# Kernel tuning notes

Measured on AMD Instinct MI355X. Metric: run time of the kernel, lower is better.

Reference implementation:

```python
import jax, jax.numpy as jnp
import numpy as np

N_NODES = 50000
N_FEAT = 128
HIDDEN = 3
N_EDGES = 600000
N_POWERS = 3


def setup_inputs() -> dict:
    key = jax.random.key(0)
    ks = jax.random.split(key, 6)
    x = jax.random.normal(ks[0], (N_NODES, N_FEAT), dtype=jnp.float32)
    edge_index = jax.random.randint(ks[1], (N_POWERS, 2, N_EDGES), 0, N_NODES, dtype=jnp.int64)
    # MLP params for the 3 adjacency powers, stacked on the leading axis.
    # torch Linear(in,out) stored transposed here: y = x @ W + b.
    Wa = jax.random.normal(ks[2], (N_POWERS, N_FEAT, HIDDEN), dtype=jnp.float32) * (1.0 / np.sqrt(N_FEAT))
    ba = jax.random.normal(ks[3], (N_POWERS, HIDDEN), dtype=jnp.float32) * 0.01
    Wb = jax.random.normal(ks[4], (N_POWERS, HIDDEN, 1), dtype=jnp.float32) * (1.0 / np.sqrt(HIDDEN))
    bb = jax.random.normal(ks[5], (N_POWERS, 1), dtype=jnp.float32) * 0.01
    return {"x": x, "edge_index": edge_index, "Wa": Wa, "ba": ba, "Wb": Wb, "bb": bb}


def reference(x, edge_index, Wa, ba, Wb, bb):
    # Gather source/target node features per edge, per adjacency power.
    x_j = x[edge_index[:, 0]]          # [P, E, F]
    x_i = x[edge_index[:, 1]]          # [P, E, F]
    abs_dif = jnp.abs(x_j - x_i)       # [P, E, F]
    # Tiny per-edge MLP: Linear -> ReLU -> Linear -> Sigmoid (separate params per power).
    h = jax.nn.relu(jnp.einsum('pef,pfh->peh', abs_dif, Wa) + ba[:, None, :])  # [P, E, H]
    w = jax.nn.sigmoid(jnp.einsum('peh,pho->peo', h, Wb) + bb[:, None, :])     # [P, E, 1]
    return w[..., 0]                   # [P, E] edge weights for each power
```

## Files before the change

kernel.cpp:

```cpp
#include <hip/hip_runtime.h>
#include <math.h>

#define N_NODES 50000
#define N_FEAT  128
#define N_EDGES 600000
#define N_POWERS 3

#define PAIRS 5
#define EDGES_PER_BLK (64 * PAIRS)

#define NB64 64
#define CAP64 10240
#define CHUNK 2048
#define NCHUNK 293

typedef _Float16 half2v __attribute__((ext_vector_type(2)));
union HU { unsigned u; half2v h; };

__device__ __forceinline__ int bj_of(int j) { return j / 6250; }

__global__ __launch_bounds__(256) void conv_x_plain(const float* __restrict__ x,
                                                    unsigned* __restrict__ xh,
                                                    const float* __restrict__ Wa,
                                                    unsigned* __restrict__ wah,
                                                    int* __restrict__ cur) {
    const int t = blockIdx.x * 256 + threadIdx.x;
    const float4* x4 = (const float4*)x;
    float4 a = x4[(size_t)t * 2];
    float4 b = x4[(size_t)t * 2 + 1];
    HU p0, p1, p2, p3;
    p0.h = half2v{(_Float16)a.x, (_Float16)a.y};
    p1.h = half2v{(_Float16)a.z, (_Float16)a.w};
    p2.h = half2v{(_Float16)b.x, (_Float16)b.y};
    p3.h = half2v{(_Float16)b.z, (_Float16)b.w};
    ((uint4*)xh)[t] = uint4{p0.u, p1.u, p2.u, p3.u};
    if (blockIdx.x == 0 && threadIdx.x < 192) {
        const int tt = threadIdx.x;
        #pragma unroll
        for (int q = 0; q < 3; ++q) {
            int idx = tt + q * 192;
            int c  = idx % 3;
            int pk = idx / 3;
            int k  = pk % 64;
            int p  = pk / 64;
            float w0 = Wa[p * 384 + (2 * k) * 3 + c];
            float w1 = Wa[p * 384 + (2 * k + 1) * 3 + c];
            HU u; u.h = half2v{(_Float16)w0, (_Float16)w1};
            wah[idx] = u.u;
        }
    }
    if (cur != nullptr && blockIdx.x == 1 && threadIdx.x < N_POWERS * NB64)
        cur[threadIdx.x] = 0;
}

__global__ __launch_bounds__(256) void scatter_onepass(const int* __restrict__ edge_index,
                                                       unsigned long long* __restrict__ su,
                                                       int* __restrict__ cur) {
    __shared__ int tot[4][NB64];
    __shared__ int sh_w[4][NB64];
    __shared__ int sh_lbase[NB64];
    __shared__ int sh_delta[NB64];
    __shared__ int sh_vt;
    __shared__ unsigned long long pay[CHUNK];
    __shared__ int dlt[CHUNK];

    const int p = blockIdx.y, chunk = blockIdx.x;
    const int tid  = threadIdx.x;
    const int lane = tid & 63;
    const int wave = tid >> 6;
    const int* ej = edge_index + (size_t)p * 2 * N_EDGES;
    const int* ei = ej + N_EDGES;
    const int base = chunk * CHUNK;

    int jj[8], ii[8], sbk[8], off[8];
    int run = 0;
    #pragma unroll
    for (int k = 0; k < 8; ++k) {
        const int e = base + k * 256 + tid;
        const bool valid = e < N_EDGES;
        jj[k] = __builtin_nontemporal_load(ej + (valid ? e : 0));
        ii[k] = __builtin_nontemporal_load(ei + (valid ? e : 0));
        const int b = bj_of(jj[k]) * 8 + bj_of(ii[k]);
        sbk[k] = b;
        const unsigned long long m0 = __ballot(b & 1);
        const unsigned long long m1 = __ballot(b & 2);
        const unsigned long long m2 = __ballot(b & 4);
        const unsigned long long m3 = __ballot(b & 8);
        const unsigned long long m4 = __ballot(b & 16);
        const unsigned long long m5 = __ballot(b & 32);
        const unsigned long long vm = __ballot(valid);
        unsigned long long m = ((b & 1) ? m0 : ~m0);
        m &= ((b & 2)  ? m1 : ~m1);
        m &= ((b & 4)  ? m2 : ~m2);
        m &= ((b & 8)  ? m3 : ~m3);
        m &= ((b & 16) ? m4 : ~m4);
        m &= ((b & 32) ? m5 : ~m5);
        m &= vm;
        const int rank = (int)__popcll(m & ((1ull << lane) - 1ull));
        unsigned long long mm = ((lane & 1) ? m0 : ~m0);
        mm &= ((lane & 2)  ? m1 : ~m1);
        mm &= ((lane & 4)  ? m2 : ~m2);
        mm &= ((lane & 8)  ? m3 : ~m3);
        mm &= ((lane & 16) ? m4 : ~m4);
        mm &= ((lane & 32) ? m5 : ~m5);
        mm &= vm;
        const int cnt = (int)__popcll(mm);
        const int pre = __shfl(run, b, 64);
        off[k] = pre + rank;
        run += cnt;
    }
    tot[wave][lane] = run;
    __syncthreads();

    if (tid < NB64) {
        const int t0 = tot[0][tid], t1 = tot[1][tid], t2 = tot[2][tid], t3 = tot[3][tid];
        const int bt = t0 + t1 + t2 + t3;
        int s = bt;
        #pragma unroll
        for (int d = 1; d < 64; d <<= 1) {
            int u = __shfl_up(s, d, 64);
            if (tid >= d) s += u;
        }
        const int lb = s - bt;
        const int g  = atomicAdd(&cur[p * NB64 + tid], bt);
        sh_lbase[tid] = lb;
        sh_delta[tid] = (p * NB64 + tid) * CAP64 + g - lb;
        sh_w[0][tid] = 0;
        sh_w[1][tid] = t0;
        sh_w[2][tid] = t0 + t1;
        sh_w[3][tid] = t0 + t1 + t2;
        if (tid == 63) sh_vt = lb + bt;
    }
    __syncthreads();

    #pragma unroll
    for (int k = 0; k < 8; ++k) {
        const int e = base + k * 256 + tid;
        if (e < N_EDGES) {
            const int b = sbk[k];
            const int pos = sh_lbase[b] + sh_w[wave][b] + off[k];
            pay[pos] = (unsigned long long)(unsigned)(jj[k] | (ii[k] << 16))
                     | ((unsigned long long)e << 32);
            dlt[pos] = sh_delta[b];
        }
    }
    __syncthreads();

    const int vt = sh_vt;
    #pragma unroll
    for (int k = 0; k < 8; ++k) {
        const int pos = k * 256 + tid;
        if (pos < vt)
            su[(size_t)(dlt[pos] + pos)] = pay[pos];
    }
}

template<int PAT>
__device__ __forceinline__ float swz(float v) {
    return __int_as_float(__builtin_amdgcn_ds_swizzle(__float_as_int(v), PAT));
}

__device__ __forceinline__ void dot3_8(const uint4& qa0, const uint4& qa1,
                                       const uint4& qb0, const uint4& qb1,
                                       const HU wa[8][3],
                                       float& h0, float& h1, float& h2) {
    unsigned ua[8] = {qa0.x, qa0.y, qa0.z, qa0.w, qa1.x, qa1.y, qa1.z, qa1.w};
    unsigned ub[8] = {qb0.x, qb0.y, qb0.z, qb0.w, qb1.x, qb1.y, qb1.z, qb1.w};
    h0 = 0.f; h1 = 0.f; h2 = 0.f;
    #pragma unroll
    for (int k = 0; k < 8; ++k) {
        HU a, b, d;
        a.u = ua[k]; b.u = ub[k];
        d.h = a.h - b.h;
        d.u &= 0x7fff7fffu;
        h0 = __builtin_amdgcn_fdot2(d.h, wa[k][0].h, h0, false);
        h1 = __builtin_amdgcn_fdot2(d.h, wa[k][1].h, h1, false);
        h2 = __builtin_amdgcn_fdot2(d.h, wa[k][2].h, h2, false);
    }
}

__global__ __launch_bounds__(256, 4) void adj_kernel_sorted(
    const unsigned* __restrict__ xh,
    const unsigned long long* __restrict__ su,
    const int* __restrict__ cur,
    const unsigned* __restrict__ wah,
    const float* __restrict__ ba,
    const float* __restrict__ Wb,
    const float* __restrict__ bb,
    float* __restrict__ out)
{
    const int p    = blockIdx.y;
    const int bj   = blockIdx.x & 7;
    const int k    = (blockIdx.x >> 3) & 31;
    const int bi   = blockIdx.x >> 8;
    const int sb   = bj * 8 + bi;
    const int tid  = threadIdx.x;
    const int lane = tid & 63;
    const int wave = tid >> 6;
    const int sub  = lane & 7;
    const int grp  = lane >> 3;

    const int count = cur[p * NB64 + sb];
    const int base  = k * EDGES_PER_BLK;
    if (base >= count) return;

    HU wa[8][3];
    {
        const unsigned* wp = wah + ((size_t)p * 64 + sub * 8) * 3;
        #pragma unroll
        for (int kk = 0; kk < 8; ++kk) {
            wa[kk][0].u = wp[kk * 3 + 0];
            wa[kk][1].u = wp[kk * 3 + 1];
            wa[kk][2].u = wp[kk * 3 + 2];
        }
        #pragma unroll
        for (int kk = 0; kk < 8; ++kk) {
            asm volatile("" : "+v"(wa[kk][0].u), "+v"(wa[kk][1].u), "+v"(wa[kk][2].u));
        }
    }

    const float ba0 = ba[p * 3 + 0], ba1 = ba[p * 3 + 1], ba2 = ba[p * 3 + 2];
    const float wb0 = Wb[p * 3 + 0], wb1 = Wb[p * 3 + 1], wb2 = Wb[p * 3 + 2];
    const float bbp = bb[p];

    const unsigned long long* sup = su + (size_t)(p * NB64 + sb) * CAP64;
    float* outp = out + (size_t)p * N_EDGES;

    const int eoff = wave * 8 + grp;
    const int roff = sub * 8;
    const int cm1  = count - 1;

    unsigned long long q[2 * PAIRS];
    #pragma unroll
    for (int it = 0; it < PAIRS; ++it) {
        const int r1 = base + it * 64 + eoff;
        q[2 * it]     = __builtin_nontemporal_load(sup + min(r1, cm1));
        q[2 * it + 1] = __builtin_nontemporal_load(sup + min(r1 + 32, cm1));
    }

    uint4 A0, A1, B0, B1, C0, C1, D0, D1;
    {
        const int j1 = (int)(q[0] & 0xFFFFu), i1 = (int)((q[0] >> 16) & 0xFFFFu);
        const int j2 = (int)(q[1] & 0xFFFFu), i2 = (int)((q[1] >> 16) & 0xFFFFu);
        const uint4* rj1 = (const uint4*)(xh + ((size_t)j1 << 6) + roff);
        const uint4* ri1 = (const uint4*)(xh + ((size_t)i1 << 6) + roff);
        const uint4* rj2 = (const uint4*)(xh + ((size_t)j2 << 6) + roff);
        const uint4* ri2 = (const uint4*)(xh + ((size_t)i2 << 6) + roff);
        A0 = rj1[0]; A1 = rj1[1]; B0 = ri1[0]; B1 = ri1[1];
        C0 = rj2[0]; C1 = rj2[1]; D0 = ri2[0]; D1 = ri2[1];
    }

    #pragma unroll
    for (int it = 0; it < PAIRS; ++it) {
        uint4 nA0, nA1, nB0, nB1, nC0, nC1, nD0, nD1;
        if (it + 1 < PAIRS) {
            const int j1 = (int)(q[2 * it + 2] & 0xFFFFu), i1 = (int)((q[2 * it + 2] >> 16) & 0xFFFFu);
            const int j2 = (int)(q[2 * it + 3] & 0xFFFFu), i2 = (int)((q[2 * it + 3] >> 16) & 0xFFFFu);
            const uint4* rj1 = (const uint4*)(xh + ((size_t)j1 << 6) + roff);
            const uint4* ri1 = (const uint4*)(xh + ((size_t)i1 << 6) + roff);
            const uint4* rj2 = (const uint4*)(xh + ((size_t)j2 << 6) + roff);
            const uint4* ri2 = (const uint4*)(xh + ((size_t)i2 << 6) + roff);
            nA0 = rj1[0]; nA1 = rj1[1]; nB0 = ri1[0]; nB1 = ri1[1];
            nC0 = rj2[0]; nC1 = rj2[1]; nD0 = ri2[0]; nD1 = ri2[1];
        }

        float h0a, h1a, h2a, h0b, h1b, h2b;
        dot3_8(A0, A1, B0, B1, wa, h0a, h1a, h2a);
        dot3_8(C0, C1, D0, D1, wa, h0b, h1b, h2b);

        h0a += swz<0x041F>(h0a); h1a += swz<0x041F>(h1a); h2a += swz<0x041F>(h2a);
        h0b += swz<0x041F>(h0b); h1b += swz<0x041F>(h1b); h2b += swz<0x041F>(h2b);
        h0a += swz<0x081F>(h0a); h1a += swz<0x081F>(h1a); h2a += swz<0x081F>(h2a);
        h0b += swz<0x081F>(h0b); h1b += swz<0x081F>(h1b); h2b += swz<0x081F>(h2b);
        h0a += swz<0x101F>(h0a); h1a += swz<0x101F>(h1a); h2a += swz<0x101F>(h2a);
        h0b += swz<0x101F>(h0b); h1b += swz<0x101F>(h1b); h2b += swz<0x101F>(h2b);

        if (sub == 0) {
            const int r1 = base + it * 64 + eoff;
            const int r2 = r1 + 32;
            if (r1 < count) {
                const int e1 = (int)(q[2 * it] >> 32);
                float r0  = fmaxf(h0a + ba0, 0.f);
                float r1f = fmaxf(h1a + ba1, 0.f);
                float r2f = fmaxf(h2a + ba2, 0.f);
                float s   = fmaf(r0, wb0, fmaf(r1f, wb1, fmaf(r2f, wb2, bbp)));
                __builtin_nontemporal_store(1.f / (1.f + __expf(-s)), outp + e1);
            }
            if (r2 < count) {
                const int e2 = (int)(q[2 * it + 1] >> 32);
                float r0  = fmaxf(h0b + ba0, 0.f);
                float r1f = fmaxf(h1b + ba1, 0.f);
                float r2f = fmaxf(h2b + ba2, 0.f);
                float s   = fmaf(r0, wb0, fmaf(r1f, wb1, fmaf(r2f, wb2, bbp)));
                __builtin_nontemporal_store(1.f / (1.f + __expf(-s)), outp + e2);
            }
        }

        if (it + 1 < PAIRS) {
            A0 = nA0; A1 = nA1; B0 = nB0; B1 = nB1;
            C0 = nC0; C1 = nC1; D0 = nD0; D1 = nD1;
        }
    }
}

__global__ __launch_bounds__(256) void adj_kernel_f16(
    const unsigned* __restrict__ xh,
    const unsigned* __restrict__ wah,
    const int*   __restrict__ edge_index,
    const float* __restrict__ ba,
    const float* __restrict__ Wb,
    const float* __restrict__ bb,
    float* __restrict__ out)
{
    const int p    = blockIdx.y;
    const int tid  = threadIdx.x;
    const int lane = tid & 63;
    const int wave = tid >> 6;
    const int sub  = lane & 7;
    const int grp  = lane >> 3;

    HU wa[8][3];
    {
        const unsigned* wp = wah + ((size_t)p * 64 + sub * 8) * 3;
        #pragma unroll
        for (int k = 0; k < 8; ++k) {
            wa[k][0].u = wp[k * 3 + 0];
            wa[k][1].u = wp[k * 3 + 1];
            wa[k][2].u = wp[k * 3 + 2];
        }
        #pragma unroll
        for (int k = 0; k < 8; ++k) {
            asm volatile("" : "+v"(wa[k][0].u), "+v"(wa[k][1].u), "+v"(wa[k][2].u));
        }
    }

    const float ba0 = ba[p * 3 + 0], ba1 = ba[p * 3 + 1], ba2 = ba[p * 3 + 2];
    const float wb0 = Wb[p * 3 + 0], wb1 = Wb[p * 3 + 1], wb2 = Wb[p * 3 + 2];
    const float bbp = bb[p];

    const int* ej = edge_index + (size_t)p * 2 * N_EDGES;
    const int* ei = ej + N_EDGES;
    float* outp = out + (size_t)p * N_EDGES;

    const int e_blk = blockIdx.x * EDGES_PER_BLK;
    const int eoff  = wave * 8 + grp;
    const int roff  = sub * 8;

    #pragma unroll
    for (int it = 0; it < PAIRS; ++it) {
        const int e1 = e_blk + it * 64 + eoff;
        const int e2 = e1 + 32;
        const int j1 = __builtin_nontemporal_load(ej + e1);
        const int i1 = __builtin_nontemporal_load(ei + e1);
        const int j2 = __builtin_nontemporal_load(ej + e2);
        const int i2 = __builtin_nontemporal_load(ei + e2);

        const uint4* rj1 = (const uint4*)(xh + ((size_t)j1 << 6) + roff);
        const uint4* ri1 = (const uint4*)(xh + ((size_t)i1 << 6) + roff);
        const uint4* rj2 = (const uint4*)(xh + ((size_t)j2 << 6) + roff);
        const uint4* ri2 = (const uint4*)(xh + ((size_t)i2 << 6) + roff);
        uint4 a0 = rj1[0], a1 = rj1[1];
        uint4 b0 = ri1[0], b1 = ri1[1];
        uint4 c0 = rj2[0], c1 = rj2[1];
        uint4 d0 = ri2[0], d1 = ri2[1];

        float h0a, h1a, h2a, h0b, h1b, h2b;
        dot3_8(a0, a1, b0, b1, wa, h0a, h1a, h2a);
        dot3_8(c0, c1, d0, d1, wa, h0b, h1b, h2b);

        h0a += swz<0x041F>(h0a); h1a += swz<0x041F>(h1a); h2a += swz<0x041F>(h2a);
        h0b += swz<0x041F>(h0b); h1b += swz<0x041F>(h1b); h2b += swz<0x041F>(h2b);
        h0a += swz<0x081F>(h0a); h1a += swz<0x081F>(h1a); h2a += swz<0x081F>(h2a);
        h0b += swz<0x081F>(h0b); h1b += swz<0x081F>(h1b); h2b += swz<0x081F>(h2b);
        h0a += swz<0x101F>(h0a); h1a += swz<0x101F>(h1a); h2a += swz<0x101F>(h2a);
        h0b += swz<0x101F>(h0b); h1b += swz<0x101F>(h1b); h2b += swz<0x101F>(h2b);

        if (sub == 0) {
            float r0 = fmaxf(h0a + ba0, 0.f);
            float r1 = fmaxf(h1a + ba1, 0.f);
            float r2 = fmaxf(h2a + ba2, 0.f);
            float s  = fmaf(r0, wb0, fmaf(r1, wb1, fmaf(r2, wb2, bbp)));
            __builtin_nontemporal_store(1.f / (1.f + __expf(-s)), outp + e1);
            r0 = fmaxf(h0b + ba0, 0.f);
            r1 = fmaxf(h1b + ba1, 0.f);
            r2 = fmaxf(h2b + ba2, 0.f);
            s  = fmaf(r0, wb0, fmaf(r1, wb1, fmaf(r2, wb2, bbp)));
            __builtin_nontemporal_store(1.f / (1.f + __expf(-s)), outp + e2);
        }
    }
}

__global__ __launch_bounds__(256) void adj_kernel_f32(
    const float* __restrict__ x,
    const int*   __restrict__ edge_index,
    const float* __restrict__ Wa,
    const float* __restrict__ ba,
    const float* __restrict__ Wb,
    const float* __restrict__ bb,
    float* __restrict__ out)
{
    const int p    = blockIdx.y;
    const int tid  = threadIdx.x;
    const int lane = tid & 63;
    const int wave = tid >> 6;
    const int sub  = lane & 15;
    const int grp  = lane >> 4;
    const int f0 = sub * 8;

    const float* Wap = Wa + (size_t)p * N_FEAT * 3;
    float wa0[8], wa1[8], wa2[8];
    #pragma unroll
    for (int k = 0; k < 8; ++k) {
        wa0[k] = Wap[(f0 + k) * 3 + 0];
        wa1[k] = Wap[(f0 + k) * 3 + 1];
        wa2[k] = Wap[(f0 + k) * 3 + 2];
    }
    const float ba0 = ba[p * 3 + 0], ba1 = ba[p * 3 + 1], ba2 = ba[p * 3 + 2];
    const float wb0 = Wb[p * 3 + 0], wb1 = Wb[p * 3 + 1], wb2 = Wb[p * 3 + 2];
    const float bbp = bb[p];

    const int e = blockIdx.x * 16 + wave * 4 + grp;
    const int* ej = edge_index + (size_t)p * 2 * N_EDGES;
    const int* ei = ej + N_EDGES;
    const int j = ej[e];
    const int i = ei[e];

    const float4* xj = (const float4*)(x + (size_t)j * N_FEAT + f0);
    const float4* xi = (const float4*)(x + (size_t)i * N_FEAT + f0);
    float4 a0 = xj[0], a1 = xj[1];
    float4 b0 = xi[0], b1 = xi[1];

    float d[8];
    d[0] = fabsf(a0.x - b0.x); d[1] = fabsf(a0.y - b0.y);
    d[2] = fabsf(a0.z - b0.z); d[3] = fabsf(a0.w - b0.w);
    d[4] = fabsf(a1.x - b1.x); d[5] = fabsf(a1.y - b1.y);
    d[6] = fabsf(a1.z - b1.z); d[7] = fabsf(a1.w - b1.w);

    float h0 = 0.f, h1 = 0.f, h2 = 0.f;
    #pragma unroll
    for (int k = 0; k < 8; ++k) {
        h0 = fmaf(d[k], wa0[k], h0);
        h1 = fmaf(d[k], wa1[k], h1);
        h2 = fmaf(d[k], wa2[k], h2);
    }
    #pragma unroll
    for (int m = 1; m < 16; m <<= 1) {
        h0 += __shfl_xor(h0, m, 64);
        h1 += __shfl_xor(h1, m, 64);
        h2 += __shfl_xor(h2, m, 64);
    }
    if (sub == 0) {
        float r0 = fmaxf(h0 + ba0, 0.f);
        float r1 = fmaxf(h1 + ba1, 0.f);
        float r2 = fmaxf(h2 + ba2, 0.f);
        float s  = fmaf(r0, wb0, fmaf(r1, wb1, fmaf(r2, wb2, bbp)));
        float w  = 1.f / (1.f + expf(-s));
        out[(size_t)p * N_EDGES + e] = w;
    }
}

extern "C" void kernel_launch(void* const* d_in, const int* in_sizes, int n_in,
                              void* d_out, int out_size, void* d_ws, size_t ws_size,
                              hipStream_t stream) {
    const float* x          = (const float*)d_in[0];
    const int*   edge_index = (const int*)d_in[1];
    const float* Wa         = (const float*)d_in[2];
    const float* ba         = (const float*)d_in[3];
    const float* Wb         = (const float*)d_in[4];
    const float* bb         = (const float*)d_in[5];
    float* out = (float*)d_out;

    const size_t x_bytes    = (size_t)N_NODES * N_FEAT * 2;
    const size_t su_bytes   = (size_t)N_POWERS * NB64 * CAP64 * 8;
    const size_t wa_bytes   = 2304;
    const size_t cur_bytes  = N_POWERS * NB64 * 4;
    const size_t need_full  = x_bytes + su_bytes + wa_bytes + cur_bytes;

    if (ws_size >= need_full) {
        char* w = (char*)d_ws;
        unsigned* xh = (unsigned*)w;
        unsigned long long* su = (unsigned long long*)(w + x_bytes);
        unsigned* wah = (unsigned*)(w + x_bytes + su_bytes);
        int* cur  = (int*)(w + x_bytes + su_bytes + wa_bytes);

        conv_x_plain<<<N_NODES * N_FEAT / 2048, 256, 0, stream>>>(x, xh, Wa, wah, cur);
        scatter_onepass<<<dim3(NCHUNK, N_POWERS), 256, 0, stream>>>(edge_index, su, cur);
        dim3 grid(NB64 * (CAP64 / EDGES_PER_BLK), N_POWERS);
        adj_kernel_sorted<<<grid, 256, 0, stream>>>(xh, su, cur, wah, ba, Wb, bb, out);
    } else if (ws_size >= x_bytes + wa_bytes) {
        unsigned* xh  = (unsigned*)d_ws;
        unsigned* wah = (unsigned*)((char*)d_ws + x_bytes);
        conv_x_plain<<<N_NODES * N_FEAT / 2048, 256, 0, stream>>>(x, xh, Wa, wah, nullptr);
        dim3 grid(N_EDGES / EDGES_PER_BLK, N_POWERS);
        adj_kernel_f16<<<grid, 256, 0, stream>>>(xh, wah, edge_index, ba, Wb, bb, out);
    } else {
        dim3 grid((N_EDGES + 15) / 16, N_POWERS);
        adj_kernel_f32<<<grid, 256, 0, stream>>>(x, edge_index, Wa, ba, Wb, bb, out);
    }
}
```

Before: 179.8 us.

## Shrink sorted edge payload to 32-bit and unscatter outputs via inverse index

The sorted edge buffer now holds only the packed (j,i) pair as 32 bits instead of 64, which halves payload traffic in the scatter and adjacency kernels. The scatter pass writes an inverse-position array per edge. The adjacency kernel writes each sigmoid result in place into the sorted slot, and a new unscatter kernel gathers those results back into original edge order with coalesced stores. This trades the random output stores for a separate inverse-index write, an extra kernel launch and a gather pass.

```diff
diff --git a/kernel.cpp b/kernel.cpp
--- a/kernel.cpp
+++ b/kernel.cpp
@@ -15,6 +15,7 @@
 #define NCHUNK 293
 
 typedef _Float16 half2v __attribute__((ext_vector_type(2)));
+typedef unsigned u32x4  __attribute__((ext_vector_type(4)));
 union HU { unsigned u; half2v h; };
 
 __device__ __forceinline__ int bj_of(int j) { return j / 6250; }
@@ -54,14 +55,15 @@
 }
 
 __global__ __launch_bounds__(256) void scatter_onepass(const int* __restrict__ edge_index,
-                                                       unsigned long long* __restrict__ su,
+                                                       unsigned* __restrict__ su,
+                                                       int* __restrict__ inv,
                                                        int* __restrict__ cur) {
     __shared__ int tot[4][NB64];
     __shared__ int sh_w[4][NB64];
     __shared__ int sh_lbase[NB64];
     __shared__ int sh_delta[NB64];
     __shared__ int sh_vt;
-    __shared__ unsigned long long pay[CHUNK];
+    __shared__ unsigned pay[CHUNK];
     __shared__ int dlt[CHUNK];
 
     const int p = blockIdx.y, chunk = blockIdx.x;
@@ -139,9 +141,9 @@
         if (e < N_EDGES) {
             const int b = sbk[k];
             const int pos = sh_lbase[b] + sh_w[wave][b] + off[k];
-            pay[pos] = (unsigned long long)(unsigned)(jj[k] | (ii[k] << 16))
-                     | ((unsigned long long)e << 32);
+            pay[pos] = (unsigned)(jj[k] | (ii[k] << 16));
             dlt[pos] = sh_delta[b];
+            inv[(size_t)p * N_EDGES + e] = sh_delta[b] + pos;
         }
     }
     __syncthreads();
@@ -160,12 +162,12 @@
     return __int_as_float(__builtin_amdgcn_ds_swizzle(__float_as_int(v), PAT));
 }
 
-__device__ __forceinline__ void dot3_8(const uint4& qa0, const uint4& qa1,
-                                       const uint4& qb0, const uint4& qb1,
+__device__ __forceinline__ void dot3_8(const u32x4& qa0, const u32x4& qa1,
+                                       const u32x4& qb0, const u32x4& qb1,
                                        const HU wa[8][3],
                                        float& h0, float& h1, float& h2) {
-    unsigned ua[8] = {qa0.x, qa0.y, qa0.z, qa0.w, qa1.x, qa1.y, qa1.z, qa1.w};
-    unsigned ub[8] = {qb0.x, qb0.y, qb0.z, qb0.w, qb1.x, qb1.y, qb1.z, qb1.w};
+    unsigned ua[8] = {qa0[0], qa0[1], qa0[2], qa0[3], qa1[0], qa1[1], qa1[2], qa1[3]};
+    unsigned ub[8] = {qb0[0], qb0[1], qb0[2], qb0[3], qb1[0], qb1[1], qb1[2], qb1[3]};
     h0 = 0.f; h1 = 0.f; h2 = 0.f;
     #pragma unroll
     for (int k = 0; k < 8; ++k) {
@@ -181,13 +183,12 @@
 
 __global__ __launch_bounds__(256, 4) void adj_kernel_sorted(
     const unsigned* __restrict__ xh,
-    const unsigned long long* __restrict__ su,
+    unsigned* su,
     const int* __restrict__ cur,
     const unsigned* __restrict__ wah,
     const float* __restrict__ ba,
     const float* __restrict__ Wb,
-    const float* __restrict__ bb,
-    float* __restrict__ out)
+    const float* __restrict__ bb)
 {
     const int p    = blockIdx.y;
     const int bj   = blockIdx.x & 7;
@@ -223,14 +224,13 @@
     const float wb0 = Wb[p * 3 + 0], wb1 = Wb[p * 3 + 1], wb2 = Wb[p * 3 + 2];
     const float bbp = bb[p];
 
-    const unsigned long long* sup = su + (size_t)(p * NB64 + sb) * CAP64;
-    float* outp = out + (size_t)p * N_EDGES;
+    unsigned* sup = su + (size_t)(p * NB64 + sb) * CAP64;
 
     const int eoff = wave * 8 + grp;
     const int roff = sub * 8;
     const int cm1  = count - 1;
 
-    unsigned long long q[2 * PAIRS];
+    unsigned q[2 * PAIRS];
     #pragma unroll
     for (int it = 0; it < PAIRS; ++it) {
         const int r1 = base + it * 64 + eoff;
@@ -238,28 +238,28 @@
         q[2 * it + 1] = __builtin_nontemporal_load(sup + min(r1 + 32, cm1));
     }
 
-    uint4 A0, A1, B0, B1, C0, C1, D0, D1;
+    u32x4 A0, A1, B0, B1, C0, C1, D0, D1;
     {
-        const int j1 = (int)(q[0] & 0xFFFFu), i1 = (int)((q[0] >> 16) & 0xFFFFu);
-        const int j2 = (int)(q[1] & 0xFFFFu), i2 = (int)((q[1] >> 16) & 0xFFFFu);
-        const uint4* rj1 = (const uint4*)(xh + ((size_t)j1 << 6) + roff);
-        const uint4* ri1 = (const uint4*)(xh + ((size_t)i1 << 6) + roff);
-        const uint4* rj2 = (const uint4*)(xh + ((size_t)j2 << 6) + roff);
-        const uint4* ri2 = (const uint4*)(xh + ((size_t)i2 << 6) + roff);
+        const int j1 = (int)(q[0] & 0xFFFFu), i1 = (int)(q[0] >> 16);
+        const int j2 = (int)(q[1] & 0xFFFFu), i2 = (int)(q[1] >> 16);
+        const u32x4* rj1 = (const u32x4*)(xh + ((size_t)j1 << 6) + roff);
+        const u32x4* ri1 = (const u32x4*)(xh + ((size_t)i1 << 6) + roff);
+        const u32x4* rj2 = (const u32x4*)(xh + ((size_t)j2 << 6) + roff);
+        const u32x4* ri2 = (const u32x4*)(xh + ((size_t)i2 << 6) + roff);
         A0 = rj1[0]; A1 = rj1[1]; B0 = ri1[0]; B1 = ri1[1];
         C0 = rj2[0]; C1 = rj2[1]; D0 = ri2[0]; D1 = ri2[1];
     }
 
     #pragma unroll
     for (int it = 0; it < PAIRS; ++it) {
-        uint4 nA0, nA1, nB0, nB1, nC0, nC1, nD0, nD1;
+        u32x4 nA0, nA1, nB0, nB1, nC0, nC1, nD0, nD1;
         if (it + 1 < PAIRS) {
-            const int j1 = (int)(q[2 * it + 2] & 0xFFFFu), i1 = (int)((q[2 * it + 2] >> 16) & 0xFFFFu);
-            const int j2 = (int)(q[2 * it + 3] & 0xFFFFu), i2 = (int)((q[2 * it + 3] >> 16) & 0xFFFFu);
-            const uint4* rj1 = (const uint4*)(xh + ((size_t)j1 << 6) + roff);
-            const uint4* ri1 = (const uint4*)(xh + ((size_t)i1 << 6) + roff);
-            const uint4* rj2 = (const uint4*)(xh + ((size_t)j2 << 6) + roff);
-            const uint4* ri2 = (const uint4*)(xh + ((size_t)i2 << 6) + roff);
+            const int j1 = (int)(q[2 * it + 2] & 0xFFFFu), i1 = (int)(q[2 * it + 2] >> 16);
+            const int j2 = (int)(q[2 * it + 3] & 0xFFFFu), i2 = (int)(q[2 * it + 3] >> 16);
+            const u32x4* rj1 = (const u32x4*)(xh + ((size_t)j1 << 6) + roff);
+            const u32x4* ri1 = (const u32x4*)(xh + ((size_t)i1 << 6) + roff);
+            const u32x4* rj2 = (const u32x4*)(xh + ((size_t)j2 << 6) + roff);
+            const u32x4* ri2 = (const u32x4*)(xh + ((size_t)i2 << 6) + roff);
             nA0 = rj1[0]; nA1 = rj1[1]; nB0 = ri1[0]; nB1 = ri1[1];
             nC0 = rj2[0]; nC1 = rj2[1]; nD0 = ri2[0]; nD1 = ri2[1];
         }
@@ -279,20 +279,18 @@
             const int r1 = base + it * 64 + eoff;
             const int r2 = r1 + 32;
             if (r1 < count) {
-                const int e1 = (int)(q[2 * it] >> 32);
                 float r0  = fmaxf(h0a + ba0, 0.f);
                 float r1f = fmaxf(h1a + ba1, 0.f);
                 float r2f = fmaxf(h2a + ba2, 0.f);
                 float s   = fmaf(r0, wb0, fmaf(r1f, wb1, fmaf(r2f, wb2, bbp)));
-                __builtin_nontemporal_store(1.f / (1.f + __expf(-s)), outp + e1);
+                ((float*)sup)[r1] = 1.f / (1.f + __expf(-s));
             }
             if (r2 < count) {
-                const int e2 = (int)(q[2 * it + 1] >> 32);
                 float r0  = fmaxf(h0b + ba0, 0.f);
                 float r1f = fmaxf(h1b + ba1, 0.f);
                 float r2f = fmaxf(h2b + ba2, 0.f);
                 float s   = fmaf(r0, wb0, fmaf(r1f, wb1, fmaf(r2f, wb2, bbp)));
-                __builtin_nontemporal_store(1.f / (1.f + __expf(-s)), outp + e2);
+                ((float*)sup)[r2] = 1.f / (1.f + __expf(-s));
             }
         }
 
@@ -301,6 +299,22 @@
             C0 = nC0; C1 = nC1; D0 = nD0; D1 = nD1;
         }
     }
+}
+
+__global__ __launch_bounds__(256) void unscatter_kernel(const unsigned* __restrict__ su,
+                                                        const int* __restrict__ inv,
+                                                        float* __restrict__ out) {
+    const int p  = blockIdx.y;
+    const int t4 = (blockIdx.x * 256 + threadIdx.x) * 4;
+    if (t4 >= N_EDGES) return;
+    const int4 iv = *(const int4*)(inv + (size_t)p * N_EDGES + t4);
+    const float* w = (const float*)su;
+    float4 o;
+    o.x = w[iv.x]; o.y = w[iv.y]; o.z = w[iv.z]; o.w = w[iv.w];
+    __builtin_nontemporal_store(o.x, out + (size_t)p * N_EDGES + t4 + 0);
+    __builtin_nontemporal_store(o.y, out + (size_t)p * N_EDGES + t4 + 1);
+    __builtin_nontemporal_store(o.z, out + (size_t)p * N_EDGES + t4 + 2);
+    __builtin_nontemporal_store(o.w, out + (size_t)p * N_EDGES + t4 + 3);
 }
 
 __global__ __launch_bounds__(256) void adj_kernel_f16(
@@ -355,14 +369,14 @@
         const int j2 = __builtin_nontemporal_load(ej + e2);
         const int i2 = __builtin_nontemporal_load(ei + e2);
 
-        const uint4* rj1 = (const uint4*)(xh + ((size_t)j1 << 6) + roff);
-        const uint4* ri1 = (const uint4*)(xh + ((size_t)i1 << 6) + roff);
-        const uint4* rj2 = (const uint4*)(xh + ((size_t)j2 << 6) + roff);
-        const uint4* ri2 = (const uint4*)(xh + ((size_t)i2 << 6) + roff);
-        uint4 a0 = rj1[0], a1 = rj1[1];
-        uint4 b0 = ri1[0], b1 = ri1[1];
-        uint4 c0 = rj2[0], c1 = rj2[1];
-        uint4 d0 = ri2[0], d1 = ri2[1];
+        const u32x4* rj1 = (const u32x4*)(xh + ((size_t)j1 << 6) + roff);
+        const u32x4* ri1 = (const u32x4*)(xh + ((size_t)i1 << 6) + roff);
+        const u32x4* rj2 = (const u32x4*)(xh + ((size_t)j2 << 6) + roff);
+        const u32x4* ri2 = (const u32x4*)(xh + ((size_t)i2 << 6) + roff);
+        u32x4 a0 = rj1[0], a1 = rj1[1];
+        u32x4 b0 = ri1[0], b1 = ri1[1];
+        u32x4 c0 = rj2[0], c1 = rj2[1];
+        u32x4 d0 = ri2[0], d1 = ri2[1];
 
         float h0a, h1a, h2a, h0b, h1b, h2b;
         dot3_8(a0, a1, b0, b1, wa, h0a, h1a, h2a);
@@ -470,23 +484,27 @@
     const float* bb         = (const float*)d_in[5];
     float* out = (float*)d_out;
 
-    const size_t x_bytes    = (size_t)N_NODES * N_FEAT * 2;
-    const size_t su_bytes   = (size_t)N_POWERS * NB64 * CAP64 * 8;
-    const size_t wa_bytes   = 2304;
-    const size_t cur_bytes  = N_POWERS * NB64 * 4;
-    const size_t need_full  = x_bytes + su_bytes + wa_bytes + cur_bytes;
+    const size_t x_bytes   = (size_t)N_NODES * N_FEAT * 2;
+    const size_t su_bytes  = (size_t)N_POWERS * NB64 * CAP64 * 4;
+    const size_t inv_bytes = (size_t)N_POWERS * N_EDGES * 4;
+    const size_t wa_bytes  = 2304;
+    const size_t cur_bytes = N_POWERS * NB64 * 4;
+    const size_t need_full = x_bytes + su_bytes + inv_bytes + wa_bytes + cur_bytes;
 
     if (ws_size >= need_full) {
         char* w = (char*)d_ws;
-        unsigned* xh = (unsigned*)w;
-        unsigned long long* su = (unsigned long long*)(w + x_bytes);
-        unsigned* wah = (unsigned*)(w + x_bytes + su_bytes);
-        int* cur  = (int*)(w + x_bytes + su_bytes + wa_bytes);
+        unsigned* xh  = (unsigned*)w;
+        unsigned* su  = (unsigned*)(w + x_bytes);
+        int*      inv = (int*)(w + x_bytes + su_bytes);
+        unsigned* wah = (unsigned*)(w + x_bytes + su_bytes + inv_bytes);
+        int*      cur = (int*)(w + x_bytes + su_bytes + inv_bytes + wa_bytes);
 
         conv_x_plain<<<N_NODES * N_FEAT / 2048, 256, 0, stream>>>(x, xh, Wa, wah, cur);
-        scatter_onepass<<<dim3(NCHUNK, N_POWERS), 256, 0, stream>>>(edge_index, su, cur);
+        scatter_onepass<<<dim3(NCHUNK, N_POWERS), 256, 0, stream>>>(edge_index, su, inv, cur);
         dim3 grid(NB64 * (CAP64 / EDGES_PER_BLK), N_POWERS);
-        adj_kernel_sorted<<<grid, 256, 0, stream>>>(xh, su, cur, wah, ba, Wb, bb, out);
+        adj_kernel_sorted<<<grid, 256, 0, stream>>>(xh, su, cur, wah, ba, Wb, bb);
+        unscatter_kernel<<<dim3((N_EDGES / 4 + 255) / 256, N_POWERS), 256, 0, stream>>>(
+            su, inv, out);
     } else if (ws_size >= x_bytes + wa_bytes) {
         unsigned* xh  = (unsigned*)d_ws;
         unsigned* wah = (unsigned*)((char*)d_ws + x_bytes);
```

New measurement: 176.8 us. About the same (-1.7%).
